# Performance work log

Measured on AMD Instinct MI355X. Metric: run time of the kernel, lower is better.

The kernel has to match this reference:

```python
import jax, jax.numpy as jnp
import numpy as np

N = 40000      # nodes
E = 640000     # edges per relation type
IN = 128; HID = 128; H2 = 64; DEC = 64; OUT = 2
T = 2          # number of edge types in edge_index_dict


def _init(k, shape, fan_in):
    return jax.random.normal(k, shape, dtype=jnp.float32) / np.sqrt(fan_in)


def setup_inputs() -> dict:
    key = jax.random.key(0)
    ks = jax.random.split(key, 16)
    return {
        "x": jax.random.normal(ks[0], (N, IN), dtype=jnp.float32),
        "edge_index_a": jax.random.randint(ks[1], (2, E), 0, N),
        "edge_index_b": jax.random.randint(ks[2], (2, E), 0, N),
        "W1": _init(ks[3], (T, IN, HID), IN),
        "a1": _init(ks[4], (T, 2, HID), HID),
        "d1_w1": _init(ks[5], (IN, DEC), IN), "d1_b1": jnp.zeros((DEC,), jnp.float32),
        "d1_w2": _init(ks[6], (DEC, T), DEC), "d1_b2": jnp.zeros((T,), jnp.float32),
        "W2": _init(ks[7], (T, HID, H2), HID),
        "a2": _init(ks[8], (T, 2, H2), H2),
        "d2_w1": _init(ks[9], (HID, DEC), HID), "d2_b1": jnp.zeros((DEC,), jnp.float32),
        "d2_w2": _init(ks[10], (DEC, T), DEC), "d2_b2": jnp.zeros((T,), jnp.float32),
        "fc1_w": _init(ks[11], (H2, HID // 4), H2), "fc1_b": jnp.zeros((HID // 4,), jnp.float32),
        "fc2_w": _init(ks[12], (HID // 4, OUT), HID // 4), "fc2_b": jnp.zeros((OUT,), jnp.float32),
    }


def _gat(x, W, a, src, dst, n):
    # single-head GAT over one edge type: gather -> edge attention -> segment softmax -> scatter
    h = x @ W                                  # [N, F]
    e = jax.nn.leaky_relu(h[src] @ a[0] + h[dst] @ a[1], 0.2)   # [E]
    m = jax.ops.segment_max(e, dst, num_segments=n)
    ex = jnp.exp(e - m[dst])
    s = jax.ops.segment_sum(ex, dst, num_segments=n)
    alpha = ex / (s[dst] + 1e-9)
    return jax.ops.segment_sum(alpha[:, None] * h[src], dst, num_segments=n)


def _dh_layer(x, edges, W, a, dw1, db1, dw2, db2):
    # decision MLP -> softmax weights over edge types; blend per-type GAT outputs
    n = x.shape[0]
    w = jax.nn.softmax(jax.nn.relu(x @ dw1 + db1) @ dw2 + db2, axis=1)  # [N, T]
    out = 0.0
    for t in range(T):
        out = out + w[:, t:t + 1] * _gat(x, W[t], a[t], edges[t][0], edges[t][1], n)
    return out


def reference(x, edge_index_a, edge_index_b, W1, a1, d1_w1, d1_b1, d1_w2, d1_b2,
              W2, a2, d2_w1, d2_b1, d2_w2, d2_b2, fc1_w, fc1_b, fc2_w, fc2_b):
    edges = (edge_index_a, edge_index_b)
    h = jax.nn.relu(_dh_layer(x, edges, W1, a1, d1_w1, d1_b1, d1_w2, d1_b2))
    h = jax.nn.relu(_dh_layer(h, edges, W2, a2, d2_w1, d2_b1, d2_w2, d2_b2))
    h = jax.nn.relu(h @ fc1_w + fc1_b)
    logits = h @ fc2_w + fc2_b
    return jax.nn.softmax(logits, axis=1)
```

## Files before the change

### kernel.cpp

```cpp
#include <hip/hip_runtime.h>
#include <hip/hip_bf16.h>

#define NN   40000
#define EE   640000
#define CAP  64


template <int M, bool BUILD>
__global__ __launch_bounds__(256) void fusedgemm_k(const float* __restrict__ X,
                                                   const float* __restrict__ WA, const float* __restrict__ WB,
                                                   const float* __restrict__ aA0, const float* __restrict__ aA1,
                                                   const float* __restrict__ aB0, const float* __restrict__ aB1,
                                                   const float* __restrict__ dw1, const float* __restrict__ db1,
                                                   const float* __restrict__ dw2, const float* __restrict__ db2,
                                                   __hip_bfloat16* __restrict__ HbA, __hip_bfloat16* __restrict__ HbB,
                                                   float* __restrict__ elA, float* __restrict__ erA,
                                                   float* __restrict__ elB, float* __restrict__ erB,
                                                   float* __restrict__ wdec,
                                                   const int* __restrict__ eiA, const int* __restrict__ eiB,
                                                   int* __restrict__ cnt, int* __restrict__ ell) {
    constexpr int K = 128;
    constexpr int NB = 16;
    constexpr int G = 256 / M;
    constexpr int R = NB / G;
    __shared__ float xs[NB][K + 4];
    __shared__ float hid[NB][65];
    __shared__ float lg[16][2];
    int n0 = blockIdx.x * NB;
    int tid = threadIdx.x;
    for (int idx = tid; idx < NB * (K / 4); idx += 256) {
        int r = idx >> 5, k4 = (idx & 31) << 2;
        *(float4*)&xs[r][k4] = *(const float4*)&X[(size_t)(n0 + r) * K + k4];
    }
    __syncthreads();

    if (BUILD) {
        int gid = blockIdx.x * 256 + tid;
        int sA = eiA[gid], dA = eiA[EE + gid];
        int cA = atomicAdd(&cnt[dA], 1);
        if (cA < CAP) ell[((size_t)dA << 6) + cA] = sA;
        int sB = eiB[gid], dB = NN + eiB[EE + gid];
        int cB = atomicAdd(&cnt[dB], 1);
        if (cB < CAP) ell[((size_t)dB << 6) + cB] = sB;
    }

    const int c = tid % M;
    const int g = tid / M;
    float accA[R], accB[R];
    #pragma unroll
    for (int r = 0; r < R; r++) { accA[r] = 0.f; accB[r] = 0.f; }
    for (int k4 = 0; k4 < K; k4 += 4) {
        float4 xv[R];
        #pragma unroll
        for (int r = 0; r < R; r++) xv[r] = *(float4*)&xs[g * R + r][k4];
        #define GSTEP(comp, kk)                                              \
        {                                                                    \
            float wA = WA[(k4 + kk) * M + c];                                \
            float wB = WB[(k4 + kk) * M + c];                                \
            _Pragma("unroll")                                                \
            for (int r = 0; r < R; r++) {                                    \
                accA[r] = fmaf(xv[r].comp, wA, accA[r]);                     \
                accB[r] = fmaf(xv[r].comp, wB, accB[r]);                     \
            }                                                                \
        }
        GSTEP(x, 0) GSTEP(y, 1) GSTEP(z, 2) GSTEP(w, 3)
        #undef GSTEP
    }

    {
        int dc = tid & 63, dg = tid >> 6;
        float da[4] = {0.f, 0.f, 0.f, 0.f};
        for (int k4 = 0; k4 < 128; k4 += 4) {
            float4 xr[4];
            #pragma unroll
            for (int r = 0; r < 4; r++) xr[r] = *(float4*)&xs[dg * 4 + r][k4];
            float w0 = dw1[(k4 + 0) * 64 + dc];
            float w1 = dw1[(k4 + 1) * 64 + dc];
            float w2 = dw1[(k4 + 2) * 64 + dc];
            float w3 = dw1[(k4 + 3) * 64 + dc];
            #pragma unroll
            for (int r = 0; r < 4; r++) {
                float s = fmaf(xr[r].x, w0, fmaf(xr[r].y, w1, fmaf(xr[r].z, w2, xr[r].w * w3)));
                da[r] += s;
            }
        }
        float b = db1[dc];
        #pragma unroll
        for (int r = 0; r < 4; r++) hid[dg * 4 + r][dc] = fmaxf(da[r] + b, 0.f);
    }
    __syncthreads();
    if (tid < 32) {
        int node = tid >> 1, o = tid & 1;
        float l = db2[o];
        #pragma unroll 4
        for (int j = 0; j < 64; j++) l += hid[node][j] * dw2[j * 2 + o];
        lg[node][o] = l;
    }
    __syncthreads();
    if (tid < 16) {
        float l0 = lg[tid][0], l1 = lg[tid][1];
        float mm = fmaxf(l0, l1);
        float e0 = __expf(l0 - mm), e1 = __expf(l1 - mm);
        float s = e0 + e1;
        wdec[(size_t)(n0 + tid) * 2 + 0] = e0 / s;
        wdec[(size_t)(n0 + tid) * 2 + 1] = e1 / s;
    }

    #pragma unroll
    for (int r = 0; r < R; r++) {
        HbA[(size_t)(n0 + g * R + r) * M + c] = __float2bfloat16(accA[r]);
        HbB[(size_t)(n0 + g * R + r) * M + c] = __float2bfloat16(accB[r]);
    }

    int row = tid >> 4, lane16 = tid & 15;
    #pragma unroll
    for (int pass = 0; pass < 4; pass++) {
        const float* av = (pass == 0) ? aA0 : (pass == 1) ? aA1 : (pass == 2) ? aB0 : aB1;
        float* dst      = (pass == 0) ? elA : (pass == 1) ? erA : (pass == 2) ? elB : erB;
        float avc = av[c];
        __syncthreads();
        #pragma unroll
        for (int r = 0; r < R; r++)
            xs[g * R + r][c] = ((pass < 2) ? accA[r] : accB[r]) * avc;
        __syncthreads();
        float s = 0.f;
        #pragma unroll
        for (int cc = lane16; cc < M; cc += 16) s += xs[row][cc];
        #pragma unroll
        for (int o = 8; o > 0; o >>= 1) s += __shfl_down(s, o, 16);
        if (lane16 == 0) dst[n0 + row] = s;
    }
}


template <int F, bool HEAD>
__global__ __launch_bounds__(256) void gat5_k(const int* __restrict__ cnt, const int* __restrict__ ell,
                                              const float* __restrict__ elA, const float* __restrict__ erA,
                                              const float* __restrict__ elB, const float* __restrict__ erB,
                                              const unsigned* __restrict__ HuA, const unsigned* __restrict__ HuB,
                                              const float* __restrict__ wdec,
                                              float* __restrict__ outF,
                                              const float* __restrict__ fc1w, const float* __restrict__ fc1b,
                                              const float* __restrict__ fc2w, const float* __restrict__ fc2b,
                                              float* __restrict__ outP, int N) {
    __shared__ uint2 se[4][CAP];
    __shared__ float hs[4][97];
    const int wid = threadIdx.x >> 6, lane = threadIdx.x & 63;
    const int n = blockIdx.x * 4 + wid;
    const int l5 = lane & 31, sub = lane >> 5;
    float acc0 = 0.f, acc1 = 0.f;

    #pragma unroll
    for (int t = 0; t < 2; t++) {
        int slot = t * N + n;
        int deg = cnt[slot];
        if (deg > CAP) deg = CAP;
        const float* el = t ? elB : elA;
        float ern = (t ? erB : erA)[n];
        const unsigned* Hu = t ? HuB : HuA;
        float coef = wdec[(size_t)n * 2 + t];
        size_t base = (size_t)slot << 6;

        int sv = 0; float ev = -1e30f;
        if (lane < deg) {
            sv = ell[base + lane];
            float e = el[sv] + ern;
            ev = (e > 0.f) ? e : 0.2f * e;
        }
        float mx = ev;
        #pragma unroll
        for (int o = 32; o > 0; o >>= 1) mx = fmaxf(mx, __shfl_xor(mx, o));
        float ex = (lane < deg) ? __expf(ev - mx) : 0.f;
        float sum = ex;
        #pragma unroll
        for (int o = 32; o > 0; o >>= 1) sum += __shfl_xor(sum, o);
        float inv = coef / (sum + 1e-9f);
        se[wid][lane] = make_uint2((unsigned)sv, __float_as_uint(ex));

        float g0 = 0.f, g1 = 0.f;
        if (F == 128) {
            int j = 0;
            for (; j + 4 <= deg; j += 4) {
                uint2 p0 = se[wid][j], p1 = se[wid][j + 1], p2 = se[wid][j + 2], p3 = se[wid][j + 3];
                unsigned h0 = Hu[(size_t)p0.x * 64 + lane];
                unsigned h1 = Hu[(size_t)p1.x * 64 + lane];
                unsigned h2 = Hu[(size_t)p2.x * 64 + lane];
                unsigned h3 = Hu[(size_t)p3.x * 64 + lane];
                float w0 = __uint_as_float(p0.y), w1 = __uint_as_float(p1.y);
                float w2 = __uint_as_float(p2.y), w3 = __uint_as_float(p3.y);
                g0 = fmaf(w0, __uint_as_float(h0 << 16), g0);
                g1 = fmaf(w0, __uint_as_float(h0 & 0xffff0000u), g1);
                g0 = fmaf(w1, __uint_as_float(h1 << 16), g0);
                g1 = fmaf(w1, __uint_as_float(h1 & 0xffff0000u), g1);
                g0 = fmaf(w2, __uint_as_float(h2 << 16), g0);
                g1 = fmaf(w2, __uint_as_float(h2 & 0xffff0000u), g1);
                g0 = fmaf(w3, __uint_as_float(h3 << 16), g0);
                g1 = fmaf(w3, __uint_as_float(h3 & 0xffff0000u), g1);
            }
            for (; j < deg; j++) {
                uint2 p = se[wid][j];
                unsigned h = Hu[(size_t)p.x * 64 + lane];
                float w = __uint_as_float(p.y);
                g0 = fmaf(w, __uint_as_float(h << 16), g0);
                g1 = fmaf(w, __uint_as_float(h & 0xffff0000u), g1);
            }
        } else {
            int j = sub;
            for (; j + 7 <= deg; j += 8) {
                uint2 p0 = se[wid][j], p1 = se[wid][j + 2], p2 = se[wid][j + 4], p3 = se[wid][j + 6];
                unsigned h0 = Hu[(size_t)p0.x * 32 + l5];
                unsigned h1 = Hu[(size_t)p1.x * 32 + l5];
                unsigned h2 = Hu[(size_t)p2.x * 32 + l5];
                unsigned h3 = Hu[(size_t)p3.x * 32 + l5];
                float w0 = __uint_as_float(p0.y), w1 = __uint_as_float(p1.y);
                float w2 = __uint_as_float(p2.y), w3 = __uint_as_float(p3.y);
                g0 = fmaf(w0, __uint_as_float(h0 << 16), g0);
                g1 = fmaf(w0, __uint_as_float(h0 & 0xffff0000u), g1);
                g0 = fmaf(w1, __uint_as_float(h1 << 16), g0);
                g1 = fmaf(w1, __uint_as_float(h1 & 0xffff0000u), g1);
                g0 = fmaf(w2, __uint_as_float(h2 << 16), g0);
                g1 = fmaf(w2, __uint_as_float(h2 & 0xffff0000u), g1);
                g0 = fmaf(w3, __uint_as_float(h3 << 16), g0);
                g1 = fmaf(w3, __uint_as_float(h3 & 0xffff0000u), g1);
            }
            for (; j < deg; j += 2) {
                uint2 p = se[wid][j];
                unsigned h = Hu[(size_t)p.x * 32 + l5];
                float w = __uint_as_float(p.y);
                g0 = fmaf(w, __uint_as_float(h << 16), g0);
                g1 = fmaf(w, __uint_as_float(h & 0xffff0000u), g1);
            }
        }
        acc0 = fmaf(inv, g0, acc0);
        acc1 = fmaf(inv, g1, acc1);
    }

    if (F == 64) {
        acc0 += __shfl_xor(acc0, 32);
        acc1 += __shfl_xor(acc1, 32);
    }

    if (!HEAD) {
        float2 v;
        v.x = fmaxf(acc0, 0.f);
        v.y = fmaxf(acc1, 0.f);
        ((float2*)outF)[(size_t)n * (F / 2) + lane] = v;
    } else {
        if (lane < 32) {
            hs[wid][2 * l5 + 0] = fmaxf(acc0, 0.f);
            hs[wid][2 * l5 + 1] = fmaxf(acc1, 0.f);
        }
        if (lane < 32) {
            float h1 = fc1b[lane];
            #pragma unroll 4
            for (int k = 0; k < 64; k++) h1 += hs[wid][k] * fc1w[k * 32 + lane];
            hs[wid][64 + lane] = fmaxf(h1, 0.f);
        }
        if (lane < 2) {
            float l = fc2b[lane];
            #pragma unroll 4
            for (int j = 0; j < 32; j++) l += hs[wid][64 + j] * fc2w[j * 2 + lane];
            float lo = __shfl(l, 0), lhi = __shfl(l, 1);
            if (lane == 0) {
                float mm = fmaxf(lo, lhi);
                float e0 = __expf(lo - mm), e1 = __expf(lhi - mm);
                float s = e0 + e1;
                float2 pr; pr.x = e0 / s; pr.y = e1 / s;
                ((float2*)outP)[n] = pr;
            }
        }
    }
}


extern "C" void kernel_launch(void* const* d_in, const int* in_sizes, int n_in,
                              void* d_out, int out_size, void* d_ws, size_t ws_size,
                              hipStream_t stream) {
    const float* x     = (const float*)d_in[0];
    const int*   eiA   = (const int*)d_in[1];
    const int*   eiB   = (const int*)d_in[2];
    const float* W1    = (const float*)d_in[3];
    const float* a1    = (const float*)d_in[4];
    const float* d1w1  = (const float*)d_in[5];
    const float* d1b1  = (const float*)d_in[6];
    const float* d1w2  = (const float*)d_in[7];
    const float* d1b2  = (const float*)d_in[8];
    const float* W2    = (const float*)d_in[9];
    const float* a2    = (const float*)d_in[10];
    const float* d2w1  = (const float*)d_in[11];
    const float* d2b1  = (const float*)d_in[12];
    const float* d2w2  = (const float*)d_in[13];
    const float* d2b2  = (const float*)d_in[14];
    const float* fc1w  = (const float*)d_in[15];
    const float* fc1b  = (const float*)d_in[16];
    const float* fc2w  = (const float*)d_in[17];
    const float* fc2b  = (const float*)d_in[18];
    float* out = (float*)d_out;

    const int N = NN;

    char* ws = (char*)d_ws;
    size_t off = 0;
    auto alloc = [&](size_t bytes) -> char* {
        char* p = ws + off;
        off = (off + bytes + 255) & ~(size_t)255;
        return p;
    };
    int*   cntAll = (int*)alloc((size_t)2 * N * sizeof(int));
    int*   ell    = (int*)alloc((size_t)2 * N * CAP * sizeof(int));
    float* wdec   = (float*)alloc((size_t)N * 2 * sizeof(float));
    float* elA    = (float*)alloc(N * sizeof(float));
    float* erA    = (float*)alloc(N * sizeof(float));
    float* elB    = (float*)alloc(N * sizeof(float));
    float* erB    = (float*)alloc(N * sizeof(float));
    __hip_bfloat16* HbA = (__hip_bfloat16*)alloc((size_t)N * 128 * sizeof(__hip_bfloat16));
    __hip_bfloat16* HbB = (__hip_bfloat16*)alloc((size_t)N * 128 * sizeof(__hip_bfloat16));
    float* hOut1  = (float*)alloc((size_t)N * 128 * sizeof(float));

    hipMemsetAsync(cntAll, 0, (size_t)2 * N * sizeof(int), stream);

    fusedgemm_k<128, true><<<N / 16, 256, 0, stream>>>(x, W1, W1 + 128 * 128,
                                                       a1, a1 + 128, a1 + 2 * 128, a1 + 3 * 128,
                                                       d1w1, d1b1, d1w2, d1b2,
                                                       HbA, HbB, elA, erA, elB, erB, wdec,
                                                       eiA, eiB, cntAll, ell);
    gat5_k<128, false><<<N / 4, 256, 0, stream>>>(cntAll, ell, elA, erA, elB, erB,
                                                  (const unsigned*)HbA, (const unsigned*)HbB,
                                                  wdec, hOut1,
                                                  nullptr, nullptr, nullptr, nullptr, nullptr, N);

    fusedgemm_k<64, false><<<N / 16, 256, 0, stream>>>(hOut1, W2, W2 + 128 * 64,
                                                       a2, a2 + 64, a2 + 2 * 64, a2 + 3 * 64,
                                                       d2w1, d2b1, d2w2, d2b2,
                                                       HbA, HbB, elA, erA, elB, erB, wdec,
                                                       nullptr, nullptr, nullptr, nullptr);
    gat5_k<64, true><<<N / 4, 256, 0, stream>>>(cntAll, ell, elA, erA, elB, erB,
                                                (const unsigned*)HbA, (const unsigned*)HbB,
                                                wdec, nullptr,
                                                fc1w, fc1b, fc2w, fc2b, out, N);
}
```

Before: 361.4 us.

## Precompute W·a vectors and compute attention logits directly from input rows

```diff
diff --git a/kernel.cpp b/kernel.cpp
--- a/kernel.cpp
+++ b/kernel.cpp
@@ -6,11 +6,32 @@
 #define CAP  64
 
 
+__global__ __launch_bounds__(256) void wa_k(const float* __restrict__ W1, const float* __restrict__ a1,
+                                            const float* __restrict__ W2, const float* __restrict__ a2,
+                                            float* __restrict__ wa) {
+    int gid = blockIdx.x * 256 + threadIdx.x;
+    int v = gid >> 7, k = gid & 127;
+    float s = 0.f;
+    if (v < 4) {
+        const float* W = W1 + (v >> 1) * 128 * 128;
+        const float* a = a1 + (v >> 1) * 2 * 128 + (v & 1) * 128;
+        #pragma unroll 4
+        for (int c = 0; c < 128; c++) s += W[k * 128 + c] * a[c];
+    } else {
+        int u = v - 4;
+        const float* W = W2 + (u >> 1) * 128 * 64;
+        const float* a = a2 + (u >> 1) * 2 * 64 + (u & 1) * 64;
+        #pragma unroll 4
+        for (int c = 0; c < 64; c++) s += W[k * 64 + c] * a[c];
+    }
+    wa[gid] = s;
+}
+
+
 template <int M, bool BUILD>
 __global__ __launch_bounds__(256) void fusedgemm_k(const float* __restrict__ X,
                                                    const float* __restrict__ WA, const float* __restrict__ WB,
-                                                   const float* __restrict__ aA0, const float* __restrict__ aA1,
-                                                   const float* __restrict__ aB0, const float* __restrict__ aB1,
+                                                   const float* __restrict__ wa,
                                                    const float* __restrict__ dw1, const float* __restrict__ db1,
                                                    const float* __restrict__ dw2, const float* __restrict__ db2,
                                                    __hip_bfloat16* __restrict__ HbA, __hip_bfloat16* __restrict__ HbB,
@@ -28,21 +49,19 @@
     __shared__ float lg[16][2];
     int n0 = blockIdx.x * NB;
     int tid = threadIdx.x;
+
     for (int idx = tid; idx < NB * (K / 4); idx += 256) {
         int r = idx >> 5, k4 = (idx & 31) << 2;
         *(float4*)&xs[r][k4] = *(const float4*)&X[(size_t)(n0 + r) * K + k4];
     }
-    __syncthreads();
-
+
+    int sA, dA, sB, dB;
     if (BUILD) {
         int gid = blockIdx.x * 256 + tid;
-        int sA = eiA[gid], dA = eiA[EE + gid];
-        int cA = atomicAdd(&cnt[dA], 1);
-        if (cA < CAP) ell[((size_t)dA << 6) + cA] = sA;
-        int sB = eiB[gid], dB = NN + eiB[EE + gid];
-        int cB = atomicAdd(&cnt[dB], 1);
-        if (cB < CAP) ell[((size_t)dB << 6) + cB] = sB;
-    }
+        sA = eiA[gid]; dA = eiA[EE + gid];
+        sB = eiB[gid]; dB = NN + eiB[EE + gid];
+    }
+    __syncthreads();
 
     const int c = tid % M;
     const int g = tid / M;
@@ -65,6 +84,12 @@
         }
         GSTEP(x, 0) GSTEP(y, 1) GSTEP(z, 2) GSTEP(w, 3)
         #undef GSTEP
+    }
+
+    int cA, cB;
+    if (BUILD) {
+        cA = atomicAdd(&cnt[dA], 1);
+        cB = atomicAdd(&cnt[dB], 1);
     }
 
     {
@@ -88,6 +113,43 @@
         #pragma unroll
         for (int r = 0; r < 4; r++) hid[dg * 4 + r][dc] = fmaxf(da[r] + b, 0.f);
     }
+
+    if (BUILD) {
+        if (cA < CAP) ell[((size_t)dA << 6) + cA] = sA;
+        if (cB < CAP) ell[((size_t)dB << 6) + cB] = sB;
+    }
+
+    {
+        int row = tid >> 4, lane16 = tid & 15;
+        float s0 = 0.f, s1 = 0.f, s2 = 0.f, s3 = 0.f;
+        #pragma unroll
+        for (int kk = 0; kk < 8; kk++) {
+            int k = lane16 + kk * 16;
+            float xv = xs[row][k];
+            s0 = fmaf(xv, wa[0 * 128 + k], s0);
+            s1 = fmaf(xv, wa[1 * 128 + k], s1);
+            s2 = fmaf(xv, wa[2 * 128 + k], s2);
+            s3 = fmaf(xv, wa[3 * 128 + k], s3);
+        }
+        #pragma unroll
+        for (int o = 8; o > 0; o >>= 1) {
+            s0 += __shfl_down(s0, o, 16);
+            s1 += __shfl_down(s1, o, 16);
+            s2 += __shfl_down(s2, o, 16);
+            s3 += __shfl_down(s3, o, 16);
+        }
+        if (lane16 == 0) {
+            elA[n0 + row] = s0; erA[n0 + row] = s1;
+            elB[n0 + row] = s2; erB[n0 + row] = s3;
+        }
+    }
+
+    #pragma unroll
+    for (int r = 0; r < R; r++) {
+        HbA[(size_t)(n0 + g * R + r) * M + c] = __float2bfloat16(accA[r]);
+        HbB[(size_t)(n0 + g * R + r) * M + c] = __float2bfloat16(accB[r]);
+    }
+
     __syncthreads();
     if (tid < 32) {
         int node = tid >> 1, o = tid & 1;
@@ -104,31 +166,6 @@
         float s = e0 + e1;
         wdec[(size_t)(n0 + tid) * 2 + 0] = e0 / s;
         wdec[(size_t)(n0 + tid) * 2 + 1] = e1 / s;
-    }
-
-    #pragma unroll
-    for (int r = 0; r < R; r++) {
-        HbA[(size_t)(n0 + g * R + r) * M + c] = __float2bfloat16(accA[r]);
-        HbB[(size_t)(n0 + g * R + r) * M + c] = __float2bfloat16(accB[r]);
-    }
-
-    int row = tid >> 4, lane16 = tid & 15;
-    #pragma unroll
-    for (int pass = 0; pass < 4; pass++) {
-        const float* av = (pass == 0) ? aA0 : (pass == 1) ? aA1 : (pass == 2) ? aB0 : aB1;
-        float* dst      = (pass == 0) ? elA : (pass == 1) ? erA : (pass == 2) ? elB : erB;
-        float avc = av[c];
-        __syncthreads();
-        #pragma unroll
-        for (int r = 0; r < R; r++)
-            xs[g * R + r][c] = ((pass < 2) ? accA[r] : accB[r]) * avc;
-        __syncthreads();
-        float s = 0.f;
-        #pragma unroll
-        for (int cc = lane16; cc < M; cc += 16) s += xs[row][cc];
-        #pragma unroll
-        for (int o = 8; o > 0; o >>= 1) s += __shfl_down(s, o, 16);
-        if (lane16 == 0) dst[n0 + row] = s;
     }
 }
 
@@ -308,6 +345,7 @@
     };
     int*   cntAll = (int*)alloc((size_t)2 * N * sizeof(int));
     int*   ell    = (int*)alloc((size_t)2 * N * CAP * sizeof(int));
+    float* wa     = (float*)alloc(8 * 128 * sizeof(float));
     float* wdec   = (float*)alloc((size_t)N * 2 * sizeof(float));
     float* elA    = (float*)alloc(N * sizeof(float));
     float* erA    = (float*)alloc(N * sizeof(float));
@@ -318,9 +356,9 @@
     float* hOut1  = (float*)alloc((size_t)N * 128 * sizeof(float));
 
     hipMemsetAsync(cntAll, 0, (size_t)2 * N * sizeof(int), stream);
-
-    fusedgemm_k<128, true><<<N / 16, 256, 0, stream>>>(x, W1, W1 + 128 * 128,
-                                                       a1, a1 + 128, a1 + 2 * 128, a1 + 3 * 128,
+    wa_k<<<4, 256, 0, stream>>>(W1, a1, W2, a2, wa);
+
+    fusedgemm_k<128, true><<<N / 16, 256, 0, stream>>>(x, W1, W1 + 128 * 128, wa,
                                                        d1w1, d1b1, d1w2, d1b2,
                                                        HbA, HbB, elA, erA, elB, erB, wdec,
                                                        eiA, eiB, cntAll, ell);
@@ -329,8 +367,7 @@
                                                   wdec, hOut1,
                                                   nullptr, nullptr, nullptr, nullptr, nullptr, N);
 
-    fusedgemm_k<64, false><<<N / 16, 256, 0, stream>>>(hOut1, W2, W2 + 128 * 64,
-                                                       a2, a2 + 64, a2 + 2 * 64, a2 + 3 * 64,
+    fusedgemm_k<64, false><<<N / 16, 256, 0, stream>>>(hOut1, W2, W2 + 128 * 64, wa + 512,
                                                        d2w1, d2b1, d2w2, d2b2,
                                                        HbA, HbB, elA, erA, elB, erB, wdec,
                                                        nullptr, nullptr, nullptr, nullptr);
```

After: 658.0 us. 82.1% more time.
